# Performance work log

Measured on AMD Instinct MI355X. Metric: run time of the kernel, lower is better.

## Reference

```python
import jax, jax.numpy as jnp
import numpy as np

ALPHA = 0.2
NEG = -9e15


def _gru(x, Wih, Whh, bih, bhh):
    # x: [B, T, F]; PyTorch nn.GRU cell equations, scan over time.
    H = Whh.shape[1]
    xg = jnp.einsum('btf,gf->btg', x, Wih) + bih  # [B,T,3H]

    def step(h, gi):
        gh = h @ Whh.T + bhh
        ir, iz, inn = jnp.split(gi, 3, axis=-1)
        hr, hz, hn = jnp.split(gh, 3, axis=-1)
        r = jax.nn.sigmoid(ir + hr)
        z = jax.nn.sigmoid(iz + hz)
        n = jnp.tanh(inn + r * hn)
        h = (1.0 - z) * n + z * h
        return h, h

    h0 = jnp.zeros((x.shape[0], H), x.dtype)
    _, ys = jax.lax.scan(step, h0, jnp.swapaxes(xg, 0, 1))
    return jnp.swapaxes(ys, 0, 1)  # [B,T,H]


def _gru_attn(x, Wih, Whh, bih, bhh, aw, ab):
    out = _gru(x, Wih, Whh, bih, bhh)              # [B,T,H]
    w = jax.nn.softmax(out @ aw + ab, axis=1)       # [B,T,1]
    return jnp.sum(out * w, axis=1)                 # [B,H]


def _gat(h, mask, W, a):
    # GraphAttentionLayer with concat=True: elu(softmax(mask(leakyrelu(Wh1+Wh2^T))) @ Wh)
    Wh = h @ W                                      # [N,O]
    O = W.shape[1]
    e = jax.nn.leaky_relu((Wh @ a[:O]) + (Wh @ a[O:]).T, ALPHA)  # [N,N]
    att = jax.nn.softmax(jnp.where(mask, e, NEG), axis=1)
    return jax.nn.elu(att @ Wh)


def setup_inputs() -> dict:
    key = jax.random.key(0)
    ks = iter(jax.random.split(key, 40))
    B, S, Wk, D, F = 1, 2048, 32, 5, 16
    H, E, NS = 128, 128, 16

    def rn(shape, scale=0.1):
        return jax.random.normal(next(ks), shape, jnp.float32) * scale

    inp = {
        'stock_features': jax.random.normal(next(ks), (B, S, Wk, D, F), jnp.float32),
        'stock_to_sector': jax.random.randint(next(ks), (S,), 0, NS, jnp.int32),
        'inter_adj': jax.random.randint(next(ks), (NS, NS), 0, 2, jnp.int32),
        'gru1_Wih': rn((3 * H, F)), 'gru1_Whh': rn((3 * H, H)),
        'gru1_bih': rn((3 * H,)), 'gru1_bhh': rn((3 * H,)),
        'attn1_w': rn((H, 1)), 'attn1_b': rn((1,)),
        'gat_intra_W': rn((H, E)), 'gat_intra_a': rn((2 * E, 1)),
        'grug_Wih': rn((3 * E, E)), 'grug_Whh': rn((3 * E, E)),
        'grug_bih': rn((3 * E,)), 'grug_bhh': rn((3 * E,)),
        'attng_w': rn((E, 1)), 'attng_b': rn((1,)),
        'grua_Wih': rn((3 * E, H)), 'grua_Whh': rn((3 * E, E)),
        'grua_bih': rn((3 * E,)), 'grua_bhh': rn((3 * E,)),
        'attna_w': rn((E, 1)), 'attna_b': rn((1,)),
        'gat_inter_W': rn((E, E)), 'gat_inter_a': rn((2 * E, 1)),
        'fusion_w': rn((3 * E, E)), 'fusion_b': rn((E,)),
        'ret_w': rn((E, 1)), 'ret_b': rn((1,)),
        'mov_w': rn((E, 1)), 'mov_b': rn((1,)),
    }
    return inp


def reference(stock_features, stock_to_sector, inter_adj,
              gru1_Wih, gru1_Whh, gru1_bih, gru1_bhh, attn1_w, attn1_b,
              gat_intra_W, gat_intra_a,
              grug_Wih, grug_Whh, grug_bih, grug_bhh, attng_w, attng_b,
              grua_Wih, grua_Whh, grua_bih, grua_bhh, attna_w, attna_b,
              gat_inter_W, gat_inter_a,
              fusion_w, fusion_b, ret_w, ret_b, mov_w, mov_b):
    B, S, Wk, D, F = stock_features.shape
    H = gru1_Whh.shape[1]
    E = gat_intra_W.shape[1]
    NS = inter_adj.shape[0]

    # Short-term: GRU-attention over days, vectorized over (batch, stock, week).
    x = stock_features.reshape(B * S * Wk, D, F)
    short = _gru_attn(x, gru1_Wih, gru1_Whh, gru1_bih, gru1_bhh, attn1_w, attn1_b)
    short = short.reshape(B, S, Wk, H)

    # Intra-sector GAT on last-week embeddings; per-sector softmax == block mask.
    same_sector = stock_to_sector[:, None] == stock_to_sector[None, :]  # [S,S]
    last = short[:, :, -1, :]                                            # [B,S,H]
    intra = jax.vmap(lambda h: _gat(h, same_sector, gat_intra_W, gat_intra_a))(last)  # [B,S,E]

    # Long-term GRU-attentions.
    lg = _gru_attn(intra.reshape(B * S, 1, E), grug_Wih, grug_Whh, grug_bih, grug_bhh,
                   attng_w, attng_b).reshape(B, S, E)
    la = _gru_attn(short.reshape(B * S, Wk, H), grua_Wih, grua_Whh, grua_bih, grua_bhh,
                   attna_w, attna_b).reshape(B, S, E)

    # Sector embeddings = mean of stock long-term embeddings per sector.
    def sector_mean(g):
        sums = jax.ops.segment_sum(g, stock_to_sector, num_segments=NS)
        cnt = jax.ops.segment_sum(jnp.ones((g.shape[0], 1), g.dtype),
                                  stock_to_sector, num_segments=NS)
        return sums / jnp.maximum(cnt, 1.0)

    sec = jax.vmap(sector_mean)(lg)                                      # [B,NS,E]
    imask = inter_adj > 0
    sec_out = jax.vmap(lambda h: _gat(h, imask, gat_inter_W, gat_inter_a))(sec)
    sec_ps = sec_out[:, stock_to_sector, :]                               # [B,S,E]

    fused = jnp.concatenate([lg, la, sec_ps], axis=-1) @ fusion_w + fusion_b
    returns = (fused @ ret_w + ret_b)[..., 0]
    moves = jax.nn.sigmoid(fused @ mov_w + mov_b)[..., 0]
    return jnp.stack([returns, moves])  # [2,B,S]
```

## Files before the change

### kernel.cpp

```cpp
#include <hip/hip_runtime.h>
#include <math.h>

#define LRELU_A 0.2f
#define NEGBIG (-9.0e15f)

typedef _Float16 f16;
typedef _Float16 f16x8 __attribute__((ext_vector_type(8)));
typedef _Float16 f16x4 __attribute__((ext_vector_type(4)));
typedef float floatx4 __attribute__((ext_vector_type(4)));

__device__ __forceinline__ float rcpf(float x){ return __builtin_amdgcn_rcpf(x); }
__device__ __forceinline__ float sigm(float x){ return rcpf(1.0f+__expf(-x)); }
__device__ __forceinline__ float gru_fuse(float xr, float xz, float xn_pre, float ghn, float h){
    float Er = __expf(-xr);
    float r  = rcpf(1.0f + Er);
    float En = __expf(2.0f*(xn_pre + r*ghn));
    float Ez = __expf(-xz);
    float Dn = En + 1.0f;
    float num = fmaf(h, Dn, (En - 1.0f)*Ez);
    float den = Dn * (1.0f + Ez);
    return num * rcpf(den);
}
__device__ __forceinline__ f16x8 load_cvt8(const float* __restrict__ p){
    float4 a = *(const float4*)p; float4 b = *(const float4*)(p+4);
    f16x8 r; r[0]=(f16)a.x; r[1]=(f16)a.y; r[2]=(f16)a.z; r[3]=(f16)a.w;
    r[4]=(f16)b.x; r[5]=(f16)b.y; r[6]=(f16)b.z; r[7]=(f16)b.w;
    return r;
}
#define MFMA16(A,B,C) __builtin_amdgcn_mfma_f32_16x16x32_f16((A),(B),(C),0,0,0)

__global__ __launch_bounds__(256) void prep_kernel(
    const float* __restrict__ g1Wih, const float* __restrict__ g1Whh,
    const float* __restrict__ gaWih, const float* __restrict__ gaWhh,
    const float* __restrict__ giW,   const float* __restrict__ fw,
    const float* __restrict__ geW,   const float* __restrict__ ggWih,
    const int* __restrict__ sec,
    f16* __restrict__ Wcat1, f16* __restrict__ WcatA,
    f16* __restrict__ WTp, f16* __restrict__ fwp, f16* __restrict__ gep,
    f16* __restrict__ ggp,
    int* __restrict__ memflat, int* __restrict__ pos,
    int* __restrict__ cnt, int* __restrict__ base)
{
    __shared__ int cs[16], wsc[16];
    const int b = blockIdx.x, tid = threadIdx.x;
    if (b < 160){
        for (int idx = b*256+tid; idx < 512*160; idx += 160*256){
            int r = idx/160, k = idx - r*160;
            float v = 0.0f;
            if (r < 256){ if (k < 32){ if (k < 16) v = g1Wih[r*16+k]; } else v = g1Whh[r*128 + (k-32)]; }
            else if (r < 384){ if (k < 16) v = g1Wih[r*16+k]; }
            else { if (k >= 32) v = g1Whh[(r-128)*128 + (k-32)]; }
            Wcat1[idx] = (f16)v;
        }
    } else if (b < 416){
        for (int idx = (b-160)*256+tid; idx < 512*256; idx += 256*256){
            int r = idx >> 8, k = idx & 255;
            float v = 0.0f;
            if (r < 256){ v = (k < 128) ? gaWih[r*128+k] : gaWhh[r*128 + (k-128)]; }
            else if (r < 384){ if (k < 128) v = gaWih[r*128+k]; }
            else { if (k >= 128) v = gaWhh[(r-128)*128 + (k-128)]; }
            WcatA[idx] = (f16)v;
        }
    } else if (b < 480){
        int idx = (b-416)*256+tid;
        int e=idx&7, lane=(idx>>3)&63, fr=idx>>9;
        int kb=fr&3, jb=fr>>2;
        int k = kb*32 + (lane>>4)*8 + e, col = jb*16 + (lane&15);
        WTp[idx] = (f16)giW[k*128 + col];
    } else if (b < 672){
        int idx = (b-480)*256+tid;
        int e=idx&7, lane=(idx>>3)&63, fr=idx>>9;
        int kb=fr%12, jb=fr/12;
        int k = kb*32 + (lane>>4)*8 + e, col = jb*16 + (lane&15);
        fwp[idx] = (f16)fw[k*128 + col];
    } else if (b < 736){
        int idx = (b-672)*256+tid;
        int e=idx&7, lane=(idx>>3)&63, fr=idx>>9;
        int kb=fr&3, jb=fr>>2;
        int k = kb*32 + (lane>>4)*8 + e, col = jb*16 + (lane&15);
        gep[idx] = (f16)geW[k*128 + col];
    } else if (b < 928){
        int idx = (b-736)*256+tid;
        int e=idx&7, lane=(idx>>3)&63, fr=idx>>9;
        int kb=fr&3, jb=(fr>>2)&7, G=fr>>5;
        int row = G*128 + jb*16 + (lane&15), k = kb*32 + (lane>>4)*8 + e;
        ggp[idx] = (f16)ggWih[row*128 + k];
    } else {
        if (tid < 16) cs[tid] = 0;
        __syncthreads();
        for (int s = tid; s < 2048; s += 256) atomicAdd(&cs[sec[s]], 1);
        __syncthreads();
        if (tid == 0){
            int acc = 0;
            for (int g=0; g<16; g++){ cnt[g]=cs[g]; base[g]=acc; wsc[g]=acc; acc+=cs[g]; }
        }
        __syncthreads();
        for (int s = tid; s < 2048; s += 256){
            int g = sec[s];
            int p = atomicAdd(&wsc[g], 1);
            memflat[p] = s;
            pos[s] = p;
        }
    }
}

__global__ __launch_bounds__(512,2) void gru_short(
    const float* __restrict__ x, const f16* __restrict__ Wcat,
    const float* __restrict__ bih, const float* __restrict__ bhh,
    const float* __restrict__ aw, const float* __restrict__ ab,
    f16* __restrict__ out)
{
    __shared__ __align__(16) f16 xs[5][32][40];
    __shared__ __align__(16) f16 hs[2][32][136];
    __shared__ float scpart[2][8][32];
    const int tid = threadIdx.x, w = tid>>6, lane = tid&63;
    const int c = lane&15, quad = lane>>4;

    { f16x4 z4 = {0,0,0,0};
      f16x4* zx = (f16x4*)&xs[0][0][0];
      for (int i=tid; i<1600; i+=512) zx[i] = z4; }

    const int jrow = w*16 + c;
    f16x8 Ar[5], Az[5], Agi, Agh[4];
#pragma unroll
    for (int kb=0;kb<5;kb++){
        Ar[kb] = *(const f16x8*)&Wcat[(size_t)(jrow)*160 + kb*32 + quad*8];
        Az[kb] = *(const f16x8*)&Wcat[(size_t)(128+jrow)*160 + kb*32 + quad*8];
    }
    Agi = *(const f16x8*)&Wcat[(size_t)(256+jrow)*160 + quad*8];
#pragma unroll
    for (int i=0;i<4;i++)
        Agh[i] = *(const f16x8*)&Wcat[(size_t)(384+jrow)*160 + 32 + i*32 + quad*8];

    float brz_r[4], brz_z[4], b_in[4], b_hn[4], awr[4];
#pragma unroll
    for (int r=0;r<4;r++){
        int j = w*16 + quad*4 + r;
        brz_r[r] = bih[j] + bhh[j];
        brz_z[r] = bih[128+j] + bhh[128+j];
        b_in[r] = bih[256+j]; b_hn[r] = bhh[256+j];
        awr[r] = aw[j];
    }
    const float abv = ab[0];

    const int s0i = tid/20,        q0 = tid - 20*s0i;
    const int i1  = tid + 512;
    const int s1i = i1/20,         q1 = i1 - 20*s1i;
    const bool pf1 = (tid < 128);
    float4 xpf0, xpf1;
    {
        const size_t base0 = (size_t)(blockIdx.x*8)*32;
        xpf0 = *(const float4*)&x[(base0 + s0i)*80 + q0*4];
        if (pf1) xpf1 = *(const float4*)&x[(base0 + s1i)*80 + q1*4];
    }

#pragma unroll 1
    for (int tile=0; tile<8; ++tile){
        const int s0 = (blockIdx.x*8 + tile)*32;
        {
            int t = (q0*4)>>4, f = (q0*4)&15;
            f16x4 h4; h4[0]=(f16)xpf0.x; h4[1]=(f16)xpf0.y; h4[2]=(f16)xpf0.z; h4[3]=(f16)xpf0.w;
            *(f16x4*)&xs[t][s0i][f] = h4;
            if (pf1){
                int t1 = (q1*4)>>4, f1 = (q1*4)&15;
                f16x4 g4; g4[0]=(f16)xpf1.x; g4[1]=(f16)xpf1.y; g4[2]=(f16)xpf1.z; g4[3]=(f16)xpf1.w;
                *(f16x4*)&xs[t1][s1i][f1] = g4;
            }
        }
        if (tile < 7){
            const size_t basen = (size_t)(s0 + 32);
            xpf0 = *(const float4*)&x[(basen + s0i)*80 + q0*4];
            if (pf1) xpf1 = *(const float4*)&x[(basen + s1i)*80 + q1*4];
        }
        float hreg[2][4], aacc[2][4], l_[2] = {0.0f, 0.0f};
#pragma unroll
        for (int st=0; st<2; st++)
#pragma unroll
            for (int r=0;r<4;r++){ aacc[st][r]=0.0f; }
        __syncthreads();

        {
            float sp[2];
#pragma unroll
            for (int st=0; st<2; st++){
                f16x8 Bx = *(const f16x8*)&xs[0][st*16+c][quad*8];
                floatx4 ar = {0,0,0,0}, az = {0,0,0,0}, agi = {0,0,0,0};
                ar = MFMA16(Ar[0], Bx, ar);
                az = MFMA16(Az[0], Bx, az);
                agi = MFMA16(Agi, Bx, agi);
                f16x4 h4;
                sp[st] = 0.0f;
#pragma unroll
                for (int r=0;r<4;r++){
                    float hn = gru_fuse(ar[r] + brz_r[r], az[r] + brz_z[r],
                                        agi[r] + b_in[r], b_hn[r], 0.0f);
                    hreg[st][r] = hn; h4[r] = (f16)hn;
                    sp[st] += hn * awr[r];
                }
                *(f16x4*)&hs[0][st*16 + c][w*16 + quad*4] = h4;
            }
#pragma unroll
            for (int st=0; st<2; st++){
                sp[st] += __shfl_xor(sp[st], 16);
                sp[st] += __shfl_xor(sp[st], 32);
            }
            if (lane < 16){ scpart[0][w][lane] = sp[0]; scpart[0][w][16+lane] = sp[1]; }
            __syncthreads();
        }

#pragma unroll 1
        for (int t=1; t<5; ++t){
            const int rp = (t&1)^1, wp = t&1;
            f16x8 Bx[2], Bh[2][4];
#pragma unroll
            for (int st=0; st<2; st++){
                Bx[st] = *(const f16x8*)&xs[t][st*16+c][quad*8];
#pragma unroll
                for (int i=0;i<4;i++)
                    Bh[st][i] = *(const f16x8*)&hs[rp][st*16+c][i*32+quad*8];
            }
            {
#pragma unroll
                for (int st=0; st<2; st++){
                    float sc = abv;
#pragma unroll
                    for (int ww=0; ww<8; ww++) sc += scpart[rp][ww][st*16+c];
                    float e = __expf(sc);
                    l_[st] += e;
#pragma unroll
                    for (int r=0;r<4;r++) aacc[st][r] += e*hreg[st][r];
                }
            }
            float sp[2];
#pragma unroll
            for (int st=0; st<2; st++){
                floatx4 ar = {0,0,0,0}, az = {0,0,0,0}, agi = {0,0,0,0}, agh = {0,0,0,0};
                ar = MFMA16(Ar[0], Bx[st], ar);
                az = MFMA16(Az[0], Bx[st], az);
                agi = MFMA16(Agi, Bx[st], agi);
#pragma unroll
                for (int i=0;i<4;i++){
                    ar = MFMA16(Ar[1+i], Bh[st][i], ar);
                    az = MFMA16(Az[1+i], Bh[st][i], az);
                    agh = MFMA16(Agh[i], Bh[st][i], agh);
                }
                f16x4 h4;
                sp[st] = 0.0f;
#pragma unroll
                for (int r=0;r<4;r++){
                    float hn = gru_fuse(ar[r] + brz_r[r], az[r] + brz_z[r],
                                        agi[r] + b_in[r], agh[r] + b_hn[r], hreg[st][r]);
                    hreg[st][r] = hn; h4[r] = (f16)hn;
                    sp[st] += hn * awr[r];
                }
                *(f16x4*)&hs[wp][st*16 + c][w*16 + quad*4] = h4;
            }
#pragma unroll
            for (int st=0; st<2; st++){
                sp[st] += __shfl_xor(sp[st], 16);
                sp[st] += __shfl_xor(sp[st], 32);
            }
            if (lane < 16){ scpart[wp][w][lane] = sp[0]; scpart[wp][w][16+lane] = sp[1]; }
            __syncthreads();
        }
#pragma unroll
        for (int st=0; st<2; st++){
            float sc = abv;
#pragma unroll
            for (int ww=0; ww<8; ww++) sc += scpart[0][ww][st*16+c];
            float e = __expf(sc);
            l_[st] += e;
            float inv = rcpf(l_[st]);
            f16x4 h4;
#pragma unroll
            for (int r=0;r<4;r++) h4[r] = (f16)((aacc[st][r] + e*hreg[st][r])*inv);
            *(f16x4*)&hs[0][st*16 + c][w*16 + quad*4] = h4;
        }
        __syncthreads();
        { int s = tid>>4, p = tid&15;
          *(f16x8*)&out[(size_t)(s0+s)*128 + p*8] = *(const f16x8*)&hs[0][s][p*8]; }
    }
}

__global__ __launch_bounds__(512,2) void gru_la_gatprep(
    const f16* __restrict__ xseq, const f16* __restrict__ Wcat,
    const float* __restrict__ bih, const float* __restrict__ bhh,
    const float* __restrict__ aw, const float* __restrict__ ab,
    f16* __restrict__ out,
    const f16* __restrict__ WTp, const float* __restrict__ gia,
    const int* __restrict__ memflat,
    f16* __restrict__ Whs, float* __restrict__ ers, float* __restrict__ el)
{
    __shared__ __align__(16) f16 xs[2][16][136];
    __shared__ __align__(16) f16 hs[2][16][136];
    __shared__ float scpart[2][8][16];
    __shared__ __align__(16) float tbuf[32][132];
    __shared__ int rows[32];
    const int tid = threadIdx.x, w = tid>>6, lane = tid&63;
    const int c = lane&15, quad = lane>>4;

    if (blockIdx.x >= 256){
        const int p0 = (blockIdx.x-256)*32;
        if (tid < 32) rows[tid] = memflat[p0 + tid];
        __syncthreads();
        f16x8 A[2][4];
#pragma unroll
        for (int mt=0;mt<2;mt++)
#pragma unroll
            for (int kb=0;kb<4;kb++)
                A[mt][kb] = *(const f16x8*)&xseq[((size_t)rows[mt*16+c]*32 + 31)*128 + kb*32 + quad*8];
        {
            f16x8 B[4];
#pragma unroll
            for (int kb=0;kb<4;kb++)
                B[kb] = *(const f16x8*)&WTp[(((size_t)(w*4+kb))*64 + lane)*8];
            floatx4 acc[2] = {{0,0,0,0},{0,0,0,0}};
#pragma unroll
            for (int kb=0;kb<4;kb++){
                acc[0] = MFMA16(A[0][kb], B[kb], acc[0]);
                acc[1] = MFMA16(A[1][kb], B[kb], acc[1]);
            }
#pragma unroll
            for (int mt=0;mt<2;mt++)
#pragma unroll
                for (int r=0;r<4;r++)
                    tbuf[mt*16 + quad*4 + r][w*16 + c] = acc[mt][r];
        }
        __syncthreads();
        for (int i=tid; i<1024; i+=512){
            int s = i>>5, p = i&31;
            float4 v = *(const float4*)&tbuf[s][p*4];
            f16x4 h4; h4[0]=(f16)v.x; h4[1]=(f16)v.y; h4[2]=(f16)v.z; h4[3]=(f16)v.w;
            *(f16x4*)&Whs[(size_t)(p0+s)*128 + p*4] = h4;
        }
        for (int k=0; k<4; k++){
            int row = w*4 + k;
            float w0 = tbuf[row][lane], w1 = tbuf[row][64+lane];
            float v1 = w0*gia[lane]     + w1*gia[64+lane];
            float v2 = w0*gia[128+lane] + w1*gia[192+lane];
#pragma unroll
            for (int off=32; off; off>>=1){ v1 += __shfl_down(v1,off); v2 += __shfl_down(v2,off); }
            if (lane==0){ el[rows[row]] = v1; ers[p0+row] = v2; }
        }
        return;
    }
    const int s0 = blockIdx.x*8;
    if (tid < 128){
        int s = tid>>4, p = tid&15;
        *(f16x8*)&xs[0][s][p*8] = *(const f16x8*)&xseq[((size_t)(s0+s)*32 + 0)*128 + p*8];
    }
    const int jrow = w*16 + c;
    f16x8 Ar[8], Az[8], Agi[4], Agh[4];
#pragma unroll
    for (int kb=0;kb<8;kb++){
        Ar[kb] = *(const f16x8*)&Wcat[(size_t)(jrow)*256 + kb*32 + quad*8];
        Az[kb] = *(const f16x8*)&Wcat[(size_t)(128+jrow)*256 + kb*32 + quad*8];
    }
#pragma unroll
    for (int i=0;i<4;i++){
        Agi[i] = *(const f16x8*)&Wcat[(size_t)(256+jrow)*256 + i*32 + quad*8];
        Agh[i] = *(const f16x8*)&Wcat[(size_t)(384+jrow)*256 + 128 + i*32 + quad*8];
    }
    float brz_r[4], brz_z[4], b_in[4], b_hn[4], awr[4];
#pragma unroll
    for (int r=0;r<4;r++){
        int j = w*16 + quad*4 + r;
        brz_r[r] = bih[j] + bhh[j];
        brz_z[r] = bih[128+j] + bhh[128+j];
        b_in[r] = bih[256+j]; b_hn[r] = bhh[256+j];
        awr[r] = aw[j];
    }
    const float abv = ab[0];
    float hreg[4] = {0,0,0,0}, aacc[4] = {0,0,0,0}, l_ = 0.0f;
    __syncthreads();

    {
        f16x8 Bx[4];
#pragma unroll
        for (int i=0;i<4;i++) Bx[i] = *(const f16x8*)&xs[0][c][i*32+quad*8];
        f16x8 xstage;
        if (tid < 128){
            int s = tid>>4, p = tid&15;
            xstage = *(const f16x8*)&xseq[((size_t)(s0+s)*32 + 1)*128 + p*8];
        }
        floatx4 ar = {0,0,0,0}, az = {0,0,0,0}, agi = {0,0,0,0};
#pragma unroll
        for (int i=0;i<4;i++){
            ar  = MFMA16(Ar[i],  Bx[i], ar);
            az  = MFMA16(Az[i],  Bx[i], az);
            agi = MFMA16(Agi[i], Bx[i], agi);
        }
        f16x4 h4;
        float sp = 0.0f;
#pragma unroll
        for (int r=0;r<4;r++){
            float hn = gru_fuse(ar[r] + brz_r[r], az[r] + brz_z[r],
                                agi[r] + b_in[r], b_hn[r], 0.0f);
            hreg[r] = hn; h4[r] = (f16)hn;
            sp += hn * awr[r];
        }
        *(f16x4*)&hs[0][c][w*16 + quad*4] = h4;
        if (tid < 128){
            int s = tid>>4, p = tid&15;
            *(f16x8*)&xs[1][s][p*8] = xstage;
        }
        sp += __shfl_xor(sp, 16);
        sp += __shfl_xor(sp, 32);
        if (lane < 16) scpart[0][w][lane] = sp;
        __syncthreads();
    }

#pragma unroll 1
    for (int t=1; t<32; ++t){
        const int rp = (t&1)^1, wp = t&1, xp = t&1;
        f16x8 Bx[4], Bh[4];
#pragma unroll
        for (int i=0;i<4;i++){
            Bx[i] = *(const f16x8*)&xs[xp][c][i*32+quad*8];
            Bh[i] = *(const f16x8*)&hs[rp][c][i*32+quad*8];
        }
        f16x8 xstage;
        const bool do_stage = (t < 31) && (tid < 128);
        if (do_stage){
            int s = tid>>4, p = tid&15;
            xstage = *(const f16x8*)&xseq[((size_t)(s0+s)*32 + t+1)*128 + p*8];
        }
        {
            float sc = abv;
#pragma unroll
            for (int ww=0; ww<8; ww++) sc += scpart[rp][ww][c];
            float e = __expf(sc);
            l_ += e;
#pragma unroll
            for (int r=0;r<4;r++) aacc[r] += e*hreg[r];
        }
        floatx4 ar = {0,0,0,0}, az = {0,0,0,0}, agi = {0,0,0,0}, agh = {0,0,0,0};
#pragma unroll
        for (int i=0;i<4;i++){
            ar = MFMA16(Ar[i], Bx[i], ar);
            az = MFMA16(Az[i], Bx[i], az);
            agi = MFMA16(Agi[i], Bx[i], agi);
        }
#pragma unroll
        for (int i=0;i<4;i++){
            ar = MFMA16(Ar[4+i], Bh[i], ar);
            az = MFMA16(Az[4+i], Bh[i], az);
            agh = MFMA16(Agh[i], Bh[i], agh);
        }
        f16x4 h4;
        float sp = 0.0f;
#pragma unroll
        for (int r=0;r<4;r++){
            float hn = gru_fuse(ar[r] + brz_r[r], az[r] + brz_z[r],
                                agi[r] + b_in[r], agh[r] + b_hn[r], hreg[r]);
            hreg[r] = hn; h4[r] = (f16)hn;
            sp += hn * awr[r];
        }
        *(f16x4*)&hs[wp][c][w*16 + quad*4] = h4;
        if (do_stage){
            int s = tid>>4, p = tid&15;
            *(f16x8*)&xs[xp^1][s][p*8] = xstage;
        }
        sp += __shfl_xor(sp, 16);
        sp += __shfl_xor(sp, 32);
        if (lane < 16) scpart[wp][w][lane] = sp;
        __syncthreads();
    }
    {
        float sc = abv;
#pragma unroll
        for (int ww=0; ww<8; ww++) sc += scpart[1][ww][c];
        float e = __expf(sc);
        l_ += e;
        float inv = rcpf(l_);
        f16x4 h4;
#pragma unroll
        for (int r=0;r<4;r++) h4[r] = (f16)((aacc[r] + e*hreg[r])*inv);
        *(f16x4*)&hs[1][c][w*16 + quad*4] = h4;
    }
    __syncthreads();
    if (tid < 128){
        int s = tid>>4, p = tid&15;
        *(f16x8*)&out[(size_t)(s0+s)*128 + p*8] = *(const f16x8*)&hs[1][s][p*8];
    }
}

__global__ __launch_bounds__(256) void gat_intra_mem_kernel(
    const f16* __restrict__ Whs, const float* __restrict__ ers,
    const float* __restrict__ el, const int* __restrict__ sec,
    const int* __restrict__ cnt, const int* __restrict__ base,
    f16* __restrict__ outp, int S)
{
    int wave = threadIdx.x>>6, lane = threadIdx.x&63;
    int i = blockIdx.x*4 + wave;
    if (i>=S) return;
    int g = sec[i];
    int n = cnt[g], b = base[g];
    float eli = el[i];
    float m = -INFINITY;
    for (int jj=lane; jj<n; jj+=64){
        float v = eli + ers[b+jj]; v = v>0.f? v : LRELU_A*v;
        m = fmaxf(m, v);
    }
#pragma unroll
    for (int off=32; off; off>>=1) m = fmaxf(m, __shfl_xor(m, off));
    float l = 0.f, c0=0.f, c1=0.f;
#pragma unroll 4
    for (int jj=0; jj<n; jj++){
        float v = eli + ers[b+jj]; v = v>0.f? v : LRELU_A*v;
        float p = __expf(v-m);
        l += p;
        c0 += p*(float)Whs[(size_t)(b+jj)*128 + lane];
        c1 += p*(float)Whs[(size_t)(b+jj)*128 + 64 + lane];
    }
    float il = rcpf(l);
    c0 *= il; c1 *= il;
    outp[(size_t)i*128+lane]    = (f16)(c0>0.f? c0 : expm1f(c0));
    outp[(size_t)i*128+64+lane] = (f16)(c1>0.f? c1 : expm1f(c1));
}

__global__ __launch_bounds__(256) void lg_mfma(
    const f16* __restrict__ intra16, const f16* __restrict__ ggp,
    const float* __restrict__ bih, const float* __restrict__ bhh,
    const int* __restrict__ pos,
    f16* __restrict__ lgout, f16* __restrict__ lgs)
{
    __shared__ __align__(16) f16 tbuf[32][136];
    const int tid = threadIdx.x, w = tid>>6, lane = tid&63;
    const int c = lane&15, quad = lane>>4;
    const int s0 = blockIdx.x*32;
    f16x8 A[2][4];
#pragma unroll
    for (int mt=0;mt<2;mt++)
#pragma unroll
        for (int kb=0;kb<4;kb++)
            A[mt][kb] = *(const f16x8*)&intra16[(size_t)(s0+mt*16+c)*128 + kb*32 + quad*8];
#pragma unroll
    for (int i=0;i<2;i++){
        int jb = w*2 + i;
        int j = jb*16 + c;
        f16x8 Br[4], Bz[4], Bn[4];
#pragma unroll
        for (int kb=0;kb<4;kb++){
            Br[kb] = *(const f16x8*)&ggp[(((size_t)((0*8+jb)*4+kb))*64 + lane)*8];
            Bz[kb] = *(const f16x8*)&ggp[(((size_t)((1*8+jb)*4+kb))*64 + lane)*8];
            Bn[kb] = *(const f16x8*)&ggp[(((size_t)((2*8+jb)*4+kb))*64 + lane)*8];
        }
        float b_r = bih[j] + bhh[j];
        float b_z = bih[128+j] + bhh[128+j];
        float b_i = bih[256+j], b_h = bhh[256+j];
        floatx4 ar[2] = {{0,0,0,0},{0,0,0,0}};
        floatx4 az[2] = {{0,0,0,0},{0,0,0,0}};
        floatx4 an[2] = {{0,0,0,0},{0,0,0,0}};
#pragma unroll
        for (int kb=0;kb<4;kb++)
#pragma unroll
            for (int mt=0;mt<2;mt++){
                ar[mt] = MFMA16(A[mt][kb], Br[kb], ar[mt]);
                az[mt] = MFMA16(A[mt][kb], Bz[kb], az[mt]);
                an[mt] = MFMA16(A[mt][kb], Bn[kb], an[mt]);
            }
#pragma unroll
        for (int mt=0;mt<2;mt++)
#pragma unroll
            for (int r=0;r<4;r++){
                float Er = __expf(-(ar[mt][r] + b_r));
                float rg = rcpf(1.0f + Er);
                float En = __expf(2.0f*(an[mt][r] + b_i + rg*b_h));
                float Ez = __expf(-(az[mt][r] + b_z));
                float v = (En - 1.0f)*Ez * rcpf((En + 1.0f)*(1.0f + Ez));
                tbuf[mt*16 + quad*4 + r][j] = (f16)v;
            }
    }
    __syncthreads();
    for (int i=tid; i<512; i+=256){
        int s = i>>4, p = i&15;
        f16x8 v = *(const f16x8*)&tbuf[s][p*8];
        *(f16x8*)&lgout[(size_t)(s0+s)*128 + p*8] = v;
        *(f16x8*)&lgs[(size_t)pos[s0+s]*128 + p*8] = v;
    }
}

__global__ __launch_bounds__(1024) void gat_inter_fused(
    const f16* __restrict__ lgs, const int* __restrict__ cnt,
    const int* __restrict__ base, const int* __restrict__ adj,
    const f16* __restrict__ gep, const float* __restrict__ a,
    float* __restrict__ outp)
{
    __shared__ __align__(16) float hs[16][132];
    __shared__ __align__(16) float Whs[16][132];
    __shared__ float el[16], er[16];
    __shared__ float att[16][16];
    const int tid = threadIdx.x, w = tid>>6, lane = tid&63;
    const int c = lane&15, quad = lane>>4;

    {
        int n = cnt[w], b = base[w];
        const int rowoff = lane>>4;
        const int colb = (lane&15)*8;
        float acc[8] = {0,0,0,0,0,0,0,0};
        for (int r = rowoff; r < n; r += 4){
            f16x8 v = *(const f16x8*)&lgs[(size_t)(b+r)*128 + colb];
#pragma unroll
            for (int k=0;k<8;k++) acc[k] += (float)v[k];
        }
#pragma unroll
        for (int k=0;k<8;k++){
            acc[k] += __shfl_xor(acc[k], 16);
            acc[k] += __shfl_xor(acc[k], 32);
        }
        if (lane < 16){
            float inv = rcpf(fmaxf((float)n, 1.0f));
#pragma unroll
            for (int k=0;k<8;k++) hs[w][colb+k] = acc[k]*inv;
        }
    }
    __syncthreads();
    if (w < 8){
        f16x8 A[4], B[4];
#pragma unroll
        for (int kb=0;kb<4;kb++){
            A[kb] = load_cvt8(&hs[c][kb*32 + quad*8]);
            B[kb] = *(const f16x8*)&gep[(((size_t)(w*4+kb))*64 + lane)*8];
        }
        floatx4 acc = {0,0,0,0};
#pragma unroll
        for (int kb=0;kb<4;kb++) acc = MFMA16(A[kb], B[kb], acc);
#pragma unroll
        for (int r=0;r<4;r++) Whs[quad*4 + r][w*16 + c] = acc[r];
    }
    __syncthreads();
    {
        int half = lane>>5, l = lane&31;
        const float* av = a + half*128;
        float acc2 = 0.f;
#pragma unroll
        for (int k=0;k<4;k++) acc2 += Whs[w][l+32*k]*av[l+32*k];
#pragma unroll
        for (int off=1; off<32; off<<=1) acc2 += __shfl_xor(acc2, off);
        if (l==0){ if (half) er[w]=acc2; else el[w]=acc2; }
    }
    __syncthreads();
    if (tid<16){
        int i=tid; float m=NEGBIG; float e[16];
        for(int j=0;j<16;j++){
            float v = el[i]+er[j]; v = v>0.f? v : LRELU_A*v;
            e[j] = (adj[i*16+j]>0)? v : NEGBIG;
            m = fmaxf(m,e[j]);
        }
        float l=0.f;
        for(int j=0;j<16;j++){ float p=__expf(e[j]-m); att[i][j]=p; l+=p; }
        float il = rcpf(l);
        for(int j=0;j<16;j++) att[i][j] *= il;
    }
    __syncthreads();
#pragma unroll
    for (int i=0;i<2;i++){
        int idx=i*1024+tid; int o=idx&127, s=idx>>7;
        float acc=0.f;
#pragma unroll
        for(int j=0;j<16;j++) acc += att[s][j]*Whs[j][o];
        outp[s*128+o] = acc>0.f? acc : expm1f(acc);
    }
}

__global__ __launch_bounds__(256) void fused_mfma(
    const f16* __restrict__ lg16, const f16* __restrict__ la16,
    const float* __restrict__ seco, const int* __restrict__ sec,
    const f16* __restrict__ fwp,
    const float* __restrict__ fb, const float* __restrict__ rw,
    const float* __restrict__ rb, const float* __restrict__ mw,
    const float* __restrict__ mb, float* __restrict__ outp)
{
    __shared__ float rpart[4][32], mpart[4][32];
    const int tid = threadIdx.x, w = tid>>6, lane = tid&63;
    const int c = lane&15, quad = lane>>4;
    const int s0 = blockIdx.x*32;
    f16x8 A[2][12];
#pragma unroll
    for (int mt=0;mt<2;mt++){
        int row = s0 + mt*16 + c;
        int g = sec[row];
#pragma unroll
        for (int kb=0;kb<4;kb++){
            A[mt][kb]   = *(const f16x8*)&lg16[(size_t)row*128 + kb*32 + quad*8];
            A[mt][4+kb] = *(const f16x8*)&la16[(size_t)row*128 + kb*32 + quad*8];
            A[mt][8+kb] = load_cvt8(&seco[(size_t)g*128 + kb*32 + quad*8]);
        }
    }
    float rsum[2][4] = {{0,0,0,0},{0,0,0,0}};
    float msum[2][4] = {{0,0,0,0},{0,0,0,0}};
#pragma unroll
    for (int i=0;i<2;i++){
        int jb = w*2 + i;
        int col = jb*16 + c;
        f16x8 B[12];
#pragma unroll
        for (int kb=0;kb<12;kb++)
            B[kb] = *(const f16x8*)&fwp[(((size_t)(jb*12+kb))*64 + lane)*8];
        floatx4 acc[2] = {{0,0,0,0},{0,0,0,0}};
#pragma unroll
        for (int kb=0;kb<12;kb++){
            acc[0] = MFMA16(A[0][kb], B[kb], acc[0]);
            acc[1] = MFMA16(A[1][kb], B[kb], acc[1]);
        }
        float fbv = fb[col], rwv = rw[col], mwv = mw[col];
#pragma unroll
        for (int mt=0;mt<2;mt++)
#pragma unroll
            for (int r=0;r<4;r++){
                float fu = acc[mt][r] + fbv;
                rsum[mt][r] += fu*rwv;
                msum[mt][r] += fu*mwv;
            }
    }
#pragma unroll
    for (int mt=0;mt<2;mt++)
#pragma unroll
        for (int r=0;r<4;r++){
#pragma unroll
            for (int off=1; off<16; off<<=1){
                rsum[mt][r] += __shfl_xor(rsum[mt][r], off);
                msum[mt][r] += __shfl_xor(msum[mt][r], off);
            }
            if (c==0){
                rpart[w][mt*16 + quad*4 + r] = rsum[mt][r];
                mpart[w][mt*16 + quad*4 + r] = msum[mt][r];
            }
        }
    __syncthreads();
    if (tid < 32){
        int s = tid;
        float rs = rb[0], ms = mb[0];
#pragma unroll
        for (int ww=0; ww<4; ww++){ rs += rpart[ww][s]; ms += mpart[ww][s]; }
        outp[s0+s] = rs;
        outp[2048 + s0 + s] = sigm(ms);
    }
}

extern "C" void kernel_launch(void* const* d_in, const int* in_sizes, int n_in,
                              void* d_out, int out_size, void* d_ws, size_t ws_size,
                              hipStream_t stream) {
    const float* sf    = (const float*)d_in[0];
    const int*   sec   = (const int*)  d_in[1];
    const int*   adj   = (const int*)  d_in[2];
    const float* g1Wih = (const float*)d_in[3];
    const float* g1Whh = (const float*)d_in[4];
    const float* g1bih = (const float*)d_in[5];
    const float* g1bhh = (const float*)d_in[6];
    const float* a1w   = (const float*)d_in[7];
    const float* a1b   = (const float*)d_in[8];
    const float* giW   = (const float*)d_in[9];
    const float* gia   = (const float*)d_in[10];
    const float* ggWih = (const float*)d_in[11];
    const float* ggbih = (const float*)d_in[13];
    const float* ggbhh = (const float*)d_in[14];
    const float* gaWih = (const float*)d_in[17];
    const float* gaWhh = (const float*)d_in[18];
    const float* gabih = (const float*)d_in[19];
    const float* gabhh = (const float*)d_in[20];
    const float* aaw   = (const float*)d_in[21];
    const float* aab   = (const float*)d_in[22];
    const float* geW   = (const float*)d_in[23];
    const float* gea   = (const float*)d_in[24];
    const float* fw    = (const float*)d_in[25];
    const float* fb    = (const float*)d_in[26];
    const float* rw    = (const float*)d_in[27];
    const float* rb    = (const float*)d_in[28];
    const float* mw    = (const float*)d_in[29];
    const float* mb    = (const float*)d_in[30];

    char* p = (char*)d_ws;
    f16*   shrt16 = (f16*)p;   p += (size_t)65536*128*2;
    f16*   intra16= (f16*)p;   p += (size_t)262144*2;
    f16*   lg16   = (f16*)p;   p += (size_t)262144*2;
    f16*   la16   = (f16*)p;   p += (size_t)262144*2;
    f16*   Whs    = (f16*)p;   p += (size_t)262144*2;
    f16*   lgs    = (f16*)p;   p += (size_t)262144*2;
    f16*   Wcat1  = (f16*)p;   p += (size_t)512*160*2;
    f16*   WcatA  = (f16*)p;   p += (size_t)512*256*2;
    f16*   WTp    = (f16*)p;   p += (size_t)16384*2;
    f16*   gep    = (f16*)p;   p += (size_t)16384*2;
    f16*   fwp    = (f16*)p;   p += (size_t)49152*2;
    f16*   ggp    = (f16*)p;   p += (size_t)49152*2;
    float* el     = (float*)p; p += 2048*4;
    float* ers    = (float*)p; p += 2048*4;
    float* seco   = (float*)p; p += 2048*4;
    int*   memflat= (int*)p;   p += 2048*4;
    int*   pos    = (int*)p;   p += 2048*4;
    int*   cnt    = (int*)p;   p += 16*4;
    int*   basep  = (int*)p;   p += 16*4;

    prep_kernel<<<929,256,0,stream>>>(g1Wih, g1Whh, gaWih, gaWhh, giW, fw, geW, ggWih, sec,
                                      Wcat1, WcatA, WTp, fwp, gep, ggp,
                                      memflat, pos, cnt, basep);
    gru_short<<<256,512,0,stream>>>(sf, Wcat1, g1bih, g1bhh, a1w, a1b, shrt16);
    gru_la_gatprep<<<320,512,0,stream>>>(shrt16, WcatA, gabih, gabhh, aaw, aab, la16,
                                         WTp, gia, memflat, Whs, ers, el);
    gat_intra_mem_kernel<<<512,256,0,stream>>>(Whs, ers, el, sec, cnt, basep, intra16, 2048);
    lg_mfma<<<64,256,0,stream>>>(intra16, ggp, ggbih, ggbhh, pos, lg16, lgs);
    gat_inter_fused<<<1,1024,0,stream>>>(lgs, cnt, basep, adj, gep, gea, seco);
    fused_mfma<<<64,256,0,stream>>>(lg16, la16, seco, sec, fwp, fb, rw, rb, mw, mb, (float*)d_out);
}
```

Before: 282.4 us.

## Overlap weight prep with short GRU kernel and store GRU outputs directly

Splits the prep kernel so only the first GRU's weight packing runs before gru_short. The rest of the weight packing and the sector bucketing move into extra blocks of the gru_short launch (769 blocks), so that work overlaps the recurrent GRU instead of running before it. The epilogues of gru_short and gru_la_gatprep now write attention-pooled outputs straight to global memory as 8-byte stores, removing a shared-memory staging pass and a barrier. The trade-off is narrower, less coalesced global stores, and prep blocks that may be scheduled ahead of GRU blocks.

```diff
diff --git a/kernel.cpp b/kernel.cpp
--- a/kernel.cpp
+++ b/kernel.cpp
@@ -29,93 +29,95 @@
 }
 #define MFMA16(A,B,C) __builtin_amdgcn_mfma_f32_16x16x32_f16((A),(B),(C),0,0,0)
 
-__global__ __launch_bounds__(256) void prep_kernel(
+__global__ __launch_bounds__(256) void prep1_kernel(
     const float* __restrict__ g1Wih, const float* __restrict__ g1Whh,
+    f16* __restrict__ Wcat1)
+{
+    const int b = blockIdx.x, tid = threadIdx.x;
+    for (int idx = b*256+tid; idx < 512*160; idx += 160*256){
+        int r = idx/160, k = idx - r*160;
+        float v = 0.0f;
+        if (r < 256){ if (k < 32){ if (k < 16) v = g1Wih[r*16+k]; } else v = g1Whh[r*128 + (k-32)]; }
+        else if (r < 384){ if (k < 16) v = g1Wih[r*16+k]; }
+        else { if (k >= 32) v = g1Whh[(r-128)*128 + (k-32)]; }
+        Wcat1[idx] = (f16)v;
+    }
+}
+
+__global__ __launch_bounds__(512,2) void gru_short(
+    const float* __restrict__ x, const f16* __restrict__ Wcat,
+    const float* __restrict__ bih, const float* __restrict__ bhh,
+    const float* __restrict__ aw, const float* __restrict__ ab,
+    f16* __restrict__ out,
     const float* __restrict__ gaWih, const float* __restrict__ gaWhh,
     const float* __restrict__ giW,   const float* __restrict__ fw,
     const float* __restrict__ geW,   const float* __restrict__ ggWih,
     const int* __restrict__ sec,
-    f16* __restrict__ Wcat1, f16* __restrict__ WcatA,
-    f16* __restrict__ WTp, f16* __restrict__ fwp, f16* __restrict__ gep,
-    f16* __restrict__ ggp,
+    f16* __restrict__ WcatA, f16* __restrict__ WTp, f16* __restrict__ fwp,
+    f16* __restrict__ gep,   f16* __restrict__ ggp,
     int* __restrict__ memflat, int* __restrict__ pos,
     int* __restrict__ cnt, int* __restrict__ base)
 {
+    __shared__ __align__(16) f16 xs[5][32][40];
+    __shared__ __align__(16) f16 hs[2][32][136];
+    __shared__ float scpart[2][8][32];
     __shared__ int cs[16], wsc[16];
-    const int b = blockIdx.x, tid = threadIdx.x;
-    if (b < 160){
-        for (int idx = b*256+tid; idx < 512*160; idx += 160*256){
-            int r = idx/160, k = idx - r*160;
-            float v = 0.0f;
-            if (r < 256){ if (k < 32){ if (k < 16) v = g1Wih[r*16+k]; } else v = g1Whh[r*128 + (k-32)]; }
-            else if (r < 384){ if (k < 16) v = g1Wih[r*16+k]; }
-            else { if (k >= 32) v = g1Whh[(r-128)*128 + (k-32)]; }
-            Wcat1[idx] = (f16)v;
-        }
-    } else if (b < 416){
-        for (int idx = (b-160)*256+tid; idx < 512*256; idx += 256*256){
+    const int tid = threadIdx.x, w = tid>>6, lane = tid&63;
+    const int c = lane&15, quad = lane>>4;
+
+    if (blockIdx.x >= 256){
+        const int b2 = blockIdx.x - 256;
+        if (b2 < 256){
+            int idx = b2*512 + tid;
             int r = idx >> 8, k = idx & 255;
             float v = 0.0f;
             if (r < 256){ v = (k < 128) ? gaWih[r*128+k] : gaWhh[r*128 + (k-128)]; }
             else if (r < 384){ if (k < 128) v = gaWih[r*128+k]; }
             else { if (k >= 128) v = gaWhh[(r-128)*128 + (k-128)]; }
             WcatA[idx] = (f16)v;
-        }
-    } else if (b < 480){
-        int idx = (b-416)*256+tid;
-        int e=idx&7, lane=(idx>>3)&63, fr=idx>>9;
-        int kb=fr&3, jb=fr>>2;
-        int k = kb*32 + (lane>>4)*8 + e, col = jb*16 + (lane&15);
-        WTp[idx] = (f16)giW[k*128 + col];
-    } else if (b < 672){
-        int idx = (b-480)*256+tid;
-        int e=idx&7, lane=(idx>>3)&63, fr=idx>>9;
-        int kb=fr%12, jb=fr/12;
-        int k = kb*32 + (lane>>4)*8 + e, col = jb*16 + (lane&15);
-        fwp[idx] = (f16)fw[k*128 + col];
-    } else if (b < 736){
-        int idx = (b-672)*256+tid;
-        int e=idx&7, lane=(idx>>3)&63, fr=idx>>9;
-        int kb=fr&3, jb=fr>>2;
-        int k = kb*32 + (lane>>4)*8 + e, col = jb*16 + (lane&15);
-        gep[idx] = (f16)geW[k*128 + col];
-    } else if (b < 928){
-        int idx = (b-736)*256+tid;
-        int e=idx&7, lane=(idx>>3)&63, fr=idx>>9;
-        int kb=fr&3, jb=(fr>>2)&7, G=fr>>5;
-        int row = G*128 + jb*16 + (lane&15), k = kb*32 + (lane>>4)*8 + e;
-        ggp[idx] = (f16)ggWih[row*128 + k];
-    } else {
-        if (tid < 16) cs[tid] = 0;
-        __syncthreads();
-        for (int s = tid; s < 2048; s += 256) atomicAdd(&cs[sec[s]], 1);
-        __syncthreads();
-        if (tid == 0){
-            int acc = 0;
-            for (int g=0; g<16; g++){ cnt[g]=cs[g]; base[g]=acc; wsc[g]=acc; acc+=cs[g]; }
-        }
-        __syncthreads();
-        for (int s = tid; s < 2048; s += 256){
-            int g = sec[s];
-            int p = atomicAdd(&wsc[g], 1);
-            memflat[p] = s;
-            pos[s] = p;
-        }
-    }
-}
-
-__global__ __launch_bounds__(512,2) void gru_short(
-    const float* __restrict__ x, const f16* __restrict__ Wcat,
-    const float* __restrict__ bih, const float* __restrict__ bhh,
-    const float* __restrict__ aw, const float* __restrict__ ab,
-    f16* __restrict__ out)
-{
-    __shared__ __align__(16) f16 xs[5][32][40];
-    __shared__ __align__(16) f16 hs[2][32][136];
-    __shared__ float scpart[2][8][32];
-    const int tid = threadIdx.x, w = tid>>6, lane = tid&63;
-    const int c = lane&15, quad = lane>>4;
-
+        } else if (b2 < 288){
+            int idx = (b2-256)*512 + tid;
+            int e=idx&7, ln=(idx>>3)&63, fr=idx>>9;
+            int kb=fr&3, jb=fr>>2;
+            int k = kb*32 + (ln>>4)*8 + e, col = jb*16 + (ln&15);
+            WTp[idx] = (f16)giW[k*128 + col];
+        } else if (b2 < 384){
+            int idx = (b2-288)*512 + tid;
+            int e=idx&7, ln=(idx>>3)&63, fr=idx>>9;
+            int kb=fr%12, jb=fr/12;
+            int k = kb*32 + (ln>>4)*8 + e, col = jb*16 + (ln&15);
+            fwp[idx] = (f16)fw[k*128 + col];
+        } else if (b2 < 416){
+            int idx = (b2-384)*512 + tid;
+            int e=idx&7, ln=(idx>>3)&63, fr=idx>>9;
+            int kb=fr&3, jb=fr>>2;
+            int k = kb*32 + (ln>>4)*8 + e, col = jb*16 + (ln&15);
+            gep[idx] = (f16)geW[k*128 + col];
+        } else if (b2 < 512){
+            int idx = (b2-416)*512 + tid;
+            int e=idx&7, ln=(idx>>3)&63, fr=idx>>9;
+            int kb=fr&3, jb=(fr>>2)&7, G=fr>>5;
+            int row = G*128 + jb*16 + (ln&15), k = kb*32 + (ln>>4)*8 + e;
+            ggp[idx] = (f16)ggWih[row*128 + k];
+        } else {
+            if (tid < 16) cs[tid] = 0;
+            __syncthreads();
+            for (int s = tid; s < 2048; s += 512) atomicAdd(&cs[sec[s]], 1);
+            __syncthreads();
+            if (tid == 0){
+                int acc = 0;
+                for (int g=0; g<16; g++){ cnt[g]=cs[g]; base[g]=acc; wsc[g]=acc; acc+=cs[g]; }
+            }
+            __syncthreads();
+            for (int s = tid; s < 2048; s += 512){
+                int g = sec[s];
+                int p2 = atomicAdd(&wsc[g], 1);
+                memflat[p2] = s;
+                pos[s] = p2;
+            }
+        }
+        return;
+    }
     { f16x4 z4 = {0,0,0,0};
       f16x4* zx = (f16x4*)&xs[0][0][0];
       for (int i=tid; i<1600; i+=512) zx[i] = z4; }
@@ -274,11 +276,8 @@
             f16x4 h4;
 #pragma unroll
             for (int r=0;r<4;r++) h4[r] = (f16)((aacc[st][r] + e*hreg[st][r])*inv);
-            *(f16x4*)&hs[0][st*16 + c][w*16 + quad*4] = h4;
-        }
-        __syncthreads();
-        { int s = tid>>4, p = tid&15;
-          *(f16x8*)&out[(size_t)(s0+s)*128 + p*8] = *(const f16x8*)&hs[0][s][p*8]; }
+            *(f16x4*)&out[(size_t)(s0 + st*16 + c)*128 + w*16 + quad*4] = h4;
+        }
     }
 }
 
@@ -476,12 +475,8 @@
         f16x4 h4;
 #pragma unroll
         for (int r=0;r<4;r++) h4[r] = (f16)((aacc[r] + e*hreg[r])*inv);
-        *(f16x4*)&hs[1][c][w*16 + quad*4] = h4;
-    }
-    __syncthreads();
-    if (tid < 128){
-        int s = tid>>4, p = tid&15;
-        *(f16x8*)&out[(size_t)(s0+s)*128 + p*8] = *(const f16x8*)&hs[1][s][p*8];
+        if (c < 8)
+            *(f16x4*)&out[(size_t)(s0 + c)*128 + w*16 + quad*4] = h4;
     }
 }
 
@@ -792,10 +787,11 @@
     int*   cnt    = (int*)p;   p += 16*4;
     int*   basep  = (int*)p;   p += 16*4;
 
-    prep_kernel<<<929,256,0,stream>>>(g1Wih, g1Whh, gaWih, gaWhh, giW, fw, geW, ggWih, sec,
-                                      Wcat1, WcatA, WTp, fwp, gep, ggp,
-                                      memflat, pos, cnt, basep);
-    gru_short<<<256,512,0,stream>>>(sf, Wcat1, g1bih, g1bhh, a1w, a1b, shrt16);
+    prep1_kernel<<<160,256,0,stream>>>(g1Wih, g1Whh, Wcat1);
+    gru_short<<<769,512,0,stream>>>(sf, Wcat1, g1bih, g1bhh, a1w, a1b, shrt16,
+                                    gaWih, gaWhh, giW, fw, geW, ggWih, sec,
+                                    WcatA, WTp, fwp, gep, ggp,
+                                    memflat, pos, cnt, basep);
     gru_la_gatprep<<<320,512,0,stream>>>(shrt16, WcatA, gabih, gabhh, aaw, aab, la16,
                                          WTp, gia, memflat, Whs, ers, el);
     gat_intra_mem_kernel<<<512,256,0,stream>>>(Whs, ers, el, sec, cnt, basep, intra16, 2048);
```

Measured after the change: 278.4 us. Within noise of the previous version (-1.4%).
